# Kernel tuning notes

Measured on AMD Instinct MI355X. Metric: run time of the kernel, lower is better.

## Reference

```python
import jax, jax.numpy as jnp
import numpy as np

HEADS = 16

def setup_inputs() -> dict:
    key = jax.random.key(0)
    ks = jax.random.split(key, 5)
    dim = 1024
    x = jax.random.normal(ks[0], (2, 2048, dim), dtype=jnp.float32)
    scale = 1.0 / np.sqrt(dim)
    Wq = jax.random.normal(ks[1], (dim, dim), dtype=jnp.float32) * scale
    Wk = jax.random.normal(ks[2], (dim, dim), dtype=jnp.float32) * scale
    Wv = jax.random.normal(ks[3], (dim, dim), dtype=jnp.float32) * scale
    Wo = jax.random.normal(ks[4], (dim, dim), dtype=jnp.float32) * scale
    return {"x": x, "Wq": Wq, "Wk": Wk, "Wv": Wv, "Wo": Wo}

def reference(x, Wq, Wk, Wv, Wo):
    b, n, dim = x.shape
    h = HEADS
    d = dim // h
    # projections: torch Linear y = x @ W.T (W is [out,in])
    def split_heads(t):
        return t.reshape(b, n, h, d).transpose(0, 2, 1, 3)  # b h n d
    q = split_heads(x @ Wq.T)
    k = split_heads(x @ Wk.T)
    v = split_heads(x @ Wv.T)
    scale = jnp.asarray(d, x.dtype) ** -0.5
    dots = jnp.einsum('bhid,bhjd->bhij', q, k) * scale
    # causal mask: positions j > i masked (triu with diagonal 1 since i == j)
    i_idx = jnp.arange(n)[:, None]
    j_idx = jnp.arange(n)[None, :]
    mask_value = -jnp.finfo(dots.dtype).max
    dots = jnp.where(j_idx > i_idx, mask_value, dots)
    attn = jax.nn.softmax(dots, axis=-1)  # dropout p=0 (eval) is identity
    out = jnp.einsum('bhij,bhjd->bhid', attn, v)
    out = out.transpose(0, 2, 1, 3).reshape(b, n, dim)
    return out @ Wo.T
```

## Files before the change

kernel.cpp:

```cpp
#include <hip/hip_runtime.h>
#include <hip/hip_bf16.h>

#define BATCH 2
#define SEQ   2048
#define DIM   1024
#define HEADS 16
#define DIMH  64
#define BK    32
#define LOG2E 1.44269504088896340736f
#define SM_SHIFT 16.0f

typedef __attribute__((ext_vector_type(8))) short short8;
typedef __attribute__((ext_vector_type(4))) short short4v;
typedef __attribute__((ext_vector_type(4))) float floatx4;

static __device__ __forceinline__ void gload_lds16(const void* g, void* l) {
    __builtin_amdgcn_global_load_lds(
        (const __attribute__((address_space(1))) void*)g,
        (__attribute__((address_space(3))) void*)l, 16, 0, 0);
}

static __device__ __forceinline__ unsigned pk_trunc(float a, float b) {
    return (__float_as_uint(b) & 0xffff0000u) | (__float_as_uint(a) >> 16);
}

__global__ __launch_bounds__(256) void conv_all(
    const float* __restrict__ x,  const float* __restrict__ Wq,
    const float* __restrict__ Wk, const float* __restrict__ Wv,
    const float* __restrict__ Wo,
    __hip_bfloat16* __restrict__ dst, __hip_bfloat16* __restrict__ dwo)
{
    const size_t NX = (size_t)BATCH * SEQ * DIM;
    const size_t NW = (size_t)DIM * DIM;
    size_t i = ((size_t)blockIdx.x * 256 + threadIdx.x) * 4;
    if (i >= NX + 4 * NW) return;
    const float* src; __hip_bfloat16* d;
    if (i < NX) { src = x + i; d = dst + i; }
    else if (i < NX + 3 * NW) {
        size_t j = i - NX;
        int w = (int)(j >> 20);
        src = ((w == 0) ? Wq : (w == 1) ? Wk : Wv) + (j & (NW - 1));
        d = dst + i;
    } else {
        size_t off = i - (NX + 3 * NW);
        src = Wo + off; d = dwo + off;
    }
    floatx4 f = *reinterpret_cast<const floatx4*>(src);
    short4v o;
    #pragma unroll
    for (int e = 0; e < 4; ++e) {
        __hip_bfloat16 t = __float2bfloat16(f[e]);
        o[e] = *reinterpret_cast<short*>(&t);
    }
    *reinterpret_cast<short4v*>(d) = o;
}

__global__ __launch_bounds__(256) void gemm_qkv(
    const __hip_bfloat16* __restrict__ xbf,
    const __hip_bfloat16* __restrict__ wbf,
    __hip_bfloat16* __restrict__ qkv)
{
    __shared__ __align__(16) short As[2][128 * BK];
    __shared__ __align__(16) short Bs[2][128 * BK];

    const int tid  = threadIdx.x;
    const int wv   = tid >> 6;
    const int lane = tid & 63;
    const int quad = lane >> 4;
    const int l16  = lane & 15;
    const int wm   = wv >> 1, wn = wv & 1;
    const int m0   = blockIdx.x * 128;
    const int n0   = blockIdx.y * 128;
    const int z    = n0 >> 10;
    __hip_bfloat16* out = qkv + (size_t)z * (BATCH * SEQ * DIM);

    const int srow = tid >> 2;
    const int scol = (tid & 3) * 8;

    floatx4 acc[4][4] = {};

#define QSTAGE(buf, k0v) do {                                                       \
    _Pragma("unroll")                                                               \
    for (int i_ = 0; i_ < 2; ++i_) {                                                \
        gload_lds16(xbf + (size_t)(m0 + srow + i_ * 64) * DIM + (k0v) + scol,       \
                    (char*)As[buf] + i_ * 4096 + wv * 1024);                        \
        gload_lds16(wbf + (size_t)(n0 + srow + i_ * 64) * DIM + (k0v) + scol,       \
                    (char*)Bs[buf] + i_ * 4096 + wv * 1024);                        \
    } } while (0)

    QSTAGE(0, 0);
    __syncthreads();

    int cur = 0;
    for (int t = 0; t < DIM / BK; ++t) {
        if (t + 1 < DIM / BK)
            QSTAGE(cur ^ 1, (t + 1) * BK);

        short8 af[4], bf[4];
        #pragma unroll
        for (int mt = 0; mt < 4; ++mt)
            af[mt] = *reinterpret_cast<const short8*>(
                &As[cur][(wm * 64 + mt * 16 + l16) * 32 + quad * 8]);
        #pragma unroll
        for (int nt = 0; nt < 4; ++nt)
            bf[nt] = *reinterpret_cast<const short8*>(
                &Bs[cur][(wn * 64 + nt * 16 + l16) * 32 + quad * 8]);
        #pragma unroll
        for (int mt = 0; mt < 4; ++mt)
            #pragma unroll
            for (int nt = 0; nt < 4; ++nt)
                acc[mt][nt] = __builtin_amdgcn_mfma_f32_16x16x32_bf16(
                    af[mt], bf[nt], acc[mt][nt], 0, 0, 0);

        __syncthreads();
        cur ^= 1;
    }
#undef QSTAGE

    const float esc = (z == 0) ? (0.125f * LOG2E) : 1.0f;
    #pragma unroll
    for (int mt = 0; mt < 4; ++mt) {
        #pragma unroll
        for (int nt = 0; nt < 4; ++nt) {
            const int n  = n0 + wn * 64 + nt * 16 + l16;
            const int hh = (n >> 6) & 15, dv = n & 63;
            #pragma unroll
            for (int r = 0; r < 4; ++r) {
                const int m  = m0 + wm * 64 + mt * 16 + quad * 4 + r;
                const int bb = m >> 11, nn = m & (SEQ - 1);
                const float v = acc[mt][nt][r] * esc;
                if (z < 2)
                    out[((size_t)(bb * HEADS + hh) * SEQ + nn) * DIMH + dv] = __float2bfloat16(v);
                else
                    out[((size_t)(bb * HEADS + hh) * DIMH + dv) * SEQ + nn] = __float2bfloat16(v);
            }
        }
    }
}

__global__ __launch_bounds__(256) void gemm_out(
    const __hip_bfloat16* __restrict__ qhs,
    const __hip_bfloat16* __restrict__ W,
    float* __restrict__ C)
{
    __shared__ __align__(16) short As[2][64 * BK];
    __shared__ __align__(16) short Bs[2][128 * BK];

    const int tid  = threadIdx.x;
    const int wv   = tid >> 6;
    const int lane = tid & 63;
    const int quad = lane >> 4;
    const int l16  = lane & 15;
    const int wn   = wv;
    const int m0   = blockIdx.x * 64;
    const int n0   = blockIdx.y * 128;

    const int srow = tid >> 2;
    const int scol = (tid & 3) * 8;

    floatx4 acc[4][2] = {};

#define OSTAGE(buf, k0v) do {                                                       \
    const int h_    = (k0v) >> 6;                                                   \
    const int koff_ = (k0v) & 63;                                                   \
    const int mA_   = m0 + srow;                                                    \
    const int bbA_  = mA_ >> 11, nnA_ = mA_ & (SEQ - 1);                            \
    gload_lds16(qhs + ((size_t)(bbA_ * HEADS + h_) * SEQ + nnA_) * DIMH + koff_ + scol, \
                (char*)As[buf] + wv * 1024);                                        \
    _Pragma("unroll")                                                               \
    for (int i_ = 0; i_ < 2; ++i_)                                                  \
        gload_lds16(W + (size_t)(n0 + srow + i_ * 64) * DIM + (k0v) + scol,         \
                    (char*)Bs[buf] + i_ * 4096 + wv * 1024);                        \
    } while (0)

    OSTAGE(0, 0);
    __syncthreads();

    int cur = 0;
    for (int t = 0; t < DIM / BK; ++t) {
        if (t + 1 < DIM / BK)
            OSTAGE(cur ^ 1, (t + 1) * BK);

        short8 af[4], bf[2];
        #pragma unroll
        for (int mt = 0; mt < 4; ++mt)
            af[mt] = *reinterpret_cast<const short8*>(
                &As[cur][(mt * 16 + l16) * 32 + quad * 8]);
        #pragma unroll
        for (int nt = 0; nt < 2; ++nt)
            bf[nt] = *reinterpret_cast<const short8*>(
                &Bs[cur][(wn * 32 + nt * 16 + l16) * 32 + quad * 8]);
        #pragma unroll
        for (int mt = 0; mt < 4; ++mt)
            #pragma unroll
            for (int nt = 0; nt < 2; ++nt)
                acc[mt][nt] = __builtin_amdgcn_mfma_f32_16x16x32_bf16(
                    af[mt], bf[nt], acc[mt][nt], 0, 0, 0);

        __syncthreads();
        cur ^= 1;
    }
#undef OSTAGE

    #pragma unroll
    for (int mt = 0; mt < 4; ++mt)
        #pragma unroll
        for (int nt = 0; nt < 2; ++nt) {
            const int n = n0 + wn * 32 + nt * 16 + l16;
            #pragma unroll
            for (int r = 0; r < 4; ++r) {
                const int m = m0 + mt * 16 + quad * 4 + r;
                C[(size_t)m * DIM + n] = acc[mt][nt][r];
            }
        }
}

__global__ __launch_bounds__(256) void attn_causal(
    __hip_bfloat16* __restrict__ qkv)
{
    __shared__ __align__(16) short kt[2][64 * 64];
    __shared__ __align__(16) short vt[2][64 * 64];
    __shared__ __align__(16) short pt[2][2][16 * 72];

    const int id    = blockIdx.x;
    const int combo = id & 31;
    const int p     = id >> 5;
    const int b     = combo >> 4;
    const int h     = combo & 15;
    const int tA = p, tB = 31 - p;
    const int nA = tA + 1;
    const int nB = tB + 1;
    const int total = nA + nB;

    const size_t hoff = (size_t)(b * HEADS + h) * SEQ * DIMH;
    const size_t one  = (size_t)BATCH * SEQ * DIM;
    __hip_bfloat16* qb        = qkv + hoff;
    const __hip_bfloat16* kb  = qkv + one + hoff;
    const __hip_bfloat16* vtg = qkv + 2 * one + hoff;

    const int tid  = threadIdx.x;
    const int wv   = tid >> 6;
    const int g    = wv >> 1;
    const int jh   = wv & 1;
    const int lane = tid & 63;
    const int quad = lane >> 4;
    const int l16  = lane & 15;
    const int xr   = l16 & 7;

    const int crow = tid >> 3;
    const int cjc  = tid & 7;
    const int coff = ((cjc ^ (crow & 7)) * 8);

    const short8 kone8 = {0x3F80, 0x3F80, 0x3F80, 0x3F80,
                          0x3F80, 0x3F80, 0x3F80, 0x3F80};

    int qbase = tA * 64 + g * 16;
    short8 aq[2][2];
    #pragma unroll
    for (int sb = 0; sb < 2; ++sb) {
        aq[sb][0] = *reinterpret_cast<const short8*>(
            qb + (size_t)(qbase + sb * 32 + l16) * DIMH + quad * 8);
        aq[sb][1] = *reinterpret_cast<const short8*>(
            qb + (size_t)(qbase + sb * 32 + l16) * DIMH + 32 + quad * 8);
    }
    floatx4 oacc[2][4] = {};
    floatx4 lsum[2] = {};

    short8 kreg[2], vreg[2];
    #pragma unroll
    for (int i = 0; i < 2; ++i) {
        const int row = crow + 32 * i;
        kreg[i] = *reinterpret_cast<const short8*>(kb + (size_t)row * DIMH + cjc * 8);
        vreg[i] = *reinterpret_cast<const short8*>(vtg + (size_t)row * SEQ + cjc * 8);
    }
    #pragma unroll
    for (int i = 0; i < 2; ++i) {
        const int row = crow + 32 * i;
        *reinterpret_cast<short8*>(&kt[0][row * 64 + coff]) = kreg[i];
        *reinterpret_cast<short8*>(&vt[0][row * 64 + coff]) = vreg[i];
    }
    __syncthreads();

    int cur = 0;
    for (int s = 0; s < total; ++s) {
        const bool lastA = (s == nA - 1);
        const int j0 = ((s < nA) ? s : s - nA) * 64;
        const bool hasn = (s + 1 < total);

        if (hasn) {
            const int s2 = s + 1;
            const int j1 = ((s2 < nA) ? s2 : s2 - nA) * 64;
            #pragma unroll
            for (int i = 0; i < 2; ++i) {
                const int row = crow + 32 * i;
                kreg[i] = *reinterpret_cast<const short8*>(kb + (size_t)(j1 + row) * DIMH + cjc * 8);
                vreg[i] = *reinterpret_cast<const short8*>(vtg + (size_t)row * SEQ + j1 + cjc * 8);
            }
        }

        floatx4 st[2][2];
        #pragma unroll
        for (int tt = 0; tt < 2; ++tt) {
            const int rw = (jh * 2 + tt) * 16 + l16;
            short8 a0 = *reinterpret_cast<const short8*>(&kt[cur][rw * 64 + (quad ^ xr) * 8]);
            short8 a1 = *reinterpret_cast<const short8*>(&kt[cur][rw * 64 + ((quad + 4) ^ xr) * 8]);
            #pragma unroll
            for (int sb = 0; sb < 2; ++sb) {
                floatx4 zz = {};
                zz         = __builtin_amdgcn_mfma_f32_16x16x32_bf16(a0, aq[sb][0], zz, 0, 0, 0);
                st[sb][tt] = __builtin_amdgcn_mfma_f32_16x16x32_bf16(a1, aq[sb][1], zz, 0, 0, 0);
            }
        }

        #pragma unroll
        for (int sb = 0; sb < 2; ++sb) {
            const int qs = qbase + sb * 32;
            if (j0 + 63 > qs) {
                const int qg = qs + l16;
                #pragma unroll
                for (int tt = 0; tt < 2; ++tt)
                    #pragma unroll
                    for (int r = 0; r < 4; ++r) {
                        const int jg = j0 + (jh * 2 + tt) * 16 + quad * 4 + r;
                        if (jg > qg) st[sb][tt][r] = -3.0e38f;
                    }
            }
        }

        #pragma unroll
        for (int sb = 0; sb < 2; ++sb)
            #pragma unroll
            for (int tt = 0; tt < 2; ++tt)
                #pragma unroll
                for (int r = 0; r < 4; ++r)
                    st[sb][tt][r] = __builtin_amdgcn_exp2f(st[sb][tt][r] - SM_SHIFT);

        short8 ph[2];
        #pragma unroll
        for (int sb = 0; sb < 2; ++sb) {
            #pragma unroll
            for (int tt = 0; tt < 2; ++tt) {
                const int t = jh * 2 + tt;
                *reinterpret_cast<unsigned*>(&pt[g][sb][l16 * 72 + t * 16 + quad * 4]) =
                    pk_trunc(st[sb][tt][0], st[sb][tt][1]);
                *reinterpret_cast<unsigned*>(&pt[g][sb][l16 * 72 + t * 16 + quad * 4 + 2]) =
                    pk_trunc(st[sb][tt][2], st[sb][tt][3]);
            }
            ph[sb] = *reinterpret_cast<const short8*>(&pt[g][sb][l16 * 72 + jh * 32 + quad * 8]);
            lsum[sb] = __builtin_amdgcn_mfma_f32_16x16x32_bf16(kone8, ph[sb], lsum[sb], 0, 0, 0);
        }

        #pragma unroll
        for (int dt = 0; dt < 4; ++dt) {
            const int rw = dt * 16 + l16;
            short8 vh = *reinterpret_cast<const short8*>(
                &vt[cur][rw * 64 + ((quad + 4 * jh) ^ xr) * 8]);
            #pragma unroll
            for (int sb = 0; sb < 2; ++sb)
                oacc[sb][dt] = __builtin_amdgcn_mfma_f32_16x16x32_bf16(
                    vh, ph[sb], oacc[sb][dt], 0, 0, 0);
        }

        if (hasn) {
            #pragma unroll
            for (int i = 0; i < 2; ++i) {
                const int row = crow + 32 * i;
                *reinterpret_cast<short8*>(&kt[cur ^ 1][row * 64 + coff]) = kreg[i];
                *reinterpret_cast<short8*>(&vt[cur ^ 1][row * 64 + coff]) = vreg[i];
            }
        }

        if (lastA || s == total - 1) {
            __syncthreads();
            float* xo = reinterpret_cast<float*>(g == 0 ? kt[cur] : vt[cur]);
            float* xl = reinterpret_cast<float*>(pt);
            if (jh == 1) {
                #pragma unroll
                for (int sb = 0; sb < 2; ++sb) {
                    #pragma unroll
                    for (int dt = 0; dt < 4; ++dt)
                        #pragma unroll
                        for (int r = 0; r < 4; ++r)
                            xo[sb * 1024 + (dt * 4 + r) * 64 + lane] = oacc[sb][dt][r];
                    xl[(g * 2 + sb) * 64 + lane] = lsum[sb][0];
                }
            }
            __syncthreads();
            if (jh == 0) {
                #pragma unroll
                for (int sb = 0; sb < 2; ++sb) {
                    const float rl = 1.0f / (lsum[sb][0] + xl[(g * 2 + sb) * 64 + lane]);
                    #pragma unroll
                    for (int dt = 0; dt < 4; ++dt)
                        #pragma unroll
                        for (int r = 0; r < 4; ++r) {
                            const float ov = oacc[sb][dt][r] +
                                             xo[sb * 1024 + (dt * 4 + r) * 64 + lane];
                            qb[(size_t)(qbase + sb * 32 + l16) * DIMH + dt * 16 + quad * 4 + r] =
                                __float2bfloat16(ov * rl);
                        }
                }
            }
            if (lastA) {
                qbase = tB * 64 + g * 16;
                #pragma unroll
                for (int sb = 0; sb < 2; ++sb) {
                    aq[sb][0] = *reinterpret_cast<const short8*>(
                        qb + (size_t)(qbase + sb * 32 + l16) * DIMH + quad * 8);
                    aq[sb][1] = *reinterpret_cast<const short8*>(
                        qb + (size_t)(qbase + sb * 32 + l16) * DIMH + 32 + quad * 8);
                    #pragma unroll
                    for (int dt = 0; dt < 4; ++dt)
                        #pragma unroll
                        for (int r = 0; r < 4; ++r) oacc[sb][dt][r] = 0.f;
                    #pragma unroll
                    for (int r = 0; r < 4; ++r) lsum[sb][r] = 0.f;
                }
            }
        }

        __syncthreads();
        cur ^= 1;
    }
}


extern "C" void kernel_launch(void* const* d_in, const int* in_sizes, int n_in,
                              void* d_out, int out_size, void* d_ws, size_t ws_size,
                              hipStream_t stream) {
    const float* x  = (const float*)d_in[0];
    const float* Wq = (const float*)d_in[1];
    const float* Wk = (const float*)d_in[2];
    const float* Wv = (const float*)d_in[3];
    const float* Wo = (const float*)d_in[4];

    __hip_bfloat16* qkv  = (__hip_bfloat16*)d_ws;
    __hip_bfloat16* wobf = (__hip_bfloat16*)((char*)d_ws + (size_t)24 * 1024 * 1024);

    __hip_bfloat16* xbf = (__hip_bfloat16*)d_out;
    __hip_bfloat16* wbf = xbf + (size_t)BATCH * SEQ * DIM;

    conv_all  <<<8192, 256, 0, stream>>>(x, Wq, Wk, Wv, Wo, xbf, wobf);
    gemm_qkv  <<<dim3((BATCH * SEQ) / 128, (3 * DIM) / 128), 256, 0, stream>>>(xbf, wbf, qkv);
    attn_causal<<<dim3(512), 256, 0, stream>>>(qkv);
    gemm_out  <<<dim3((BATCH * SEQ) / 64, DIM / 128), 256, 0, stream>>>(qkv, wobf, (float*)d_out);
}
```

Before: 187.5 us.

## Split paired causal attention tiles into one block per query tile

The attention kernel previously paired query tiles p and 31-p in one block to balance causal work, processing both sequentially. It now launches one block per query tile (1024 blocks), ordered longest-first, and uses pointer increments for the K/V prefetch addresses. Masking runs only on the diagonal step, and the cross-wave reduction moves out of the loop. This doubles parallelism and removes the mid-loop reset and reload, at the cost of uneven per-block work that relies on the hardware scheduler for balance.

```diff
diff --git a/kernel.cpp b/kernel.cpp
--- a/kernel.cpp
+++ b/kernel.cpp
@@ -224,13 +224,10 @@
 
     const int id    = blockIdx.x;
     const int combo = id & 31;
-    const int p     = id >> 5;
     const int b     = combo >> 4;
     const int h     = combo & 15;
-    const int tA = p, tB = 31 - p;
-    const int nA = tA + 1;
-    const int nB = tB + 1;
-    const int total = nA + nB;
+    const int tile  = 31 - (id >> 5);
+    const int total = tile + 1;
 
     const size_t hoff = (size_t)(b * HEADS + h) * SEQ * DIMH;
     const size_t one  = (size_t)BATCH * SEQ * DIM;
@@ -254,7 +251,7 @@
     const short8 kone8 = {0x3F80, 0x3F80, 0x3F80, 0x3F80,
                           0x3F80, 0x3F80, 0x3F80, 0x3F80};
 
-    int qbase = tA * 64 + g * 16;
+    const int qbase = tile * 64 + g * 16;
     short8 aq[2][2];
     #pragma unroll
     for (int sb = 0; sb < 2; ++sb) {
@@ -266,36 +263,35 @@
     floatx4 oacc[2][4] = {};
     floatx4 lsum[2] = {};
 
+    const __hip_bfloat16* kp0 = kb + (size_t)crow * DIMH + cjc * 8;
+    const __hip_bfloat16* kp1 = kb + (size_t)(crow + 32) * DIMH + cjc * 8;
+    const __hip_bfloat16* vp0 = vtg + (size_t)crow * SEQ + cjc * 8;
+    const __hip_bfloat16* vp1 = vtg + (size_t)(crow + 32) * SEQ + cjc * 8;
+
     short8 kreg[2], vreg[2];
-    #pragma unroll
-    for (int i = 0; i < 2; ++i) {
-        const int row = crow + 32 * i;
-        kreg[i] = *reinterpret_cast<const short8*>(kb + (size_t)row * DIMH + cjc * 8);
-        vreg[i] = *reinterpret_cast<const short8*>(vtg + (size_t)row * SEQ + cjc * 8);
-    }
-    #pragma unroll
-    for (int i = 0; i < 2; ++i) {
-        const int row = crow + 32 * i;
-        *reinterpret_cast<short8*>(&kt[0][row * 64 + coff]) = kreg[i];
-        *reinterpret_cast<short8*>(&vt[0][row * 64 + coff]) = vreg[i];
-    }
+    kreg[0] = *reinterpret_cast<const short8*>(kp0);
+    kreg[1] = *reinterpret_cast<const short8*>(kp1);
+    vreg[0] = *reinterpret_cast<const short8*>(vp0);
+    vreg[1] = *reinterpret_cast<const short8*>(vp1);
+    kp0 += 64 * DIMH; kp1 += 64 * DIMH; vp0 += 64; vp1 += 64;
+
+    *reinterpret_cast<short8*>(&kt[0][crow * 64 + coff])        = kreg[0];
+    *reinterpret_cast<short8*>(&kt[0][(crow + 32) * 64 + coff]) = kreg[1];
+    *reinterpret_cast<short8*>(&vt[0][crow * 64 + coff])        = vreg[0];
+    *reinterpret_cast<short8*>(&vt[0][(crow + 32) * 64 + coff]) = vreg[1];
     __syncthreads();
 
     int cur = 0;
     for (int s = 0; s < total; ++s) {
-        const bool lastA = (s == nA - 1);
-        const int j0 = ((s < nA) ? s : s - nA) * 64;
+        const int j0 = s * 64;
         const bool hasn = (s + 1 < total);
 
         if (hasn) {
-            const int s2 = s + 1;
-            const int j1 = ((s2 < nA) ? s2 : s2 - nA) * 64;
-            #pragma unroll
-            for (int i = 0; i < 2; ++i) {
-                const int row = crow + 32 * i;
-                kreg[i] = *reinterpret_cast<const short8*>(kb + (size_t)(j1 + row) * DIMH + cjc * 8);
-                vreg[i] = *reinterpret_cast<const short8*>(vtg + (size_t)row * SEQ + j1 + cjc * 8);
-            }
+            kreg[0] = *reinterpret_cast<const short8*>(kp0);
+            kreg[1] = *reinterpret_cast<const short8*>(kp1);
+            vreg[0] = *reinterpret_cast<const short8*>(vp0);
+            vreg[1] = *reinterpret_cast<const short8*>(vp1);
+            kp0 += 64 * DIMH; kp1 += 64 * DIMH; vp0 += 64; vp1 += 64;
         }
 
         floatx4 st[2][2];
@@ -312,11 +308,10 @@
             }
         }
 
-        #pragma unroll
-        for (int sb = 0; sb < 2; ++sb) {
-            const int qs = qbase + sb * 32;
-            if (j0 + 63 > qs) {
-                const int qg = qs + l16;
+        if (s == total - 1) {
+            #pragma unroll
+            for (int sb = 0; sb < 2; ++sb) {
+                const int qg = qbase + sb * 32 + l16;
                 #pragma unroll
                 for (int tt = 0; tt < 2; ++tt)
                     #pragma unroll
@@ -362,65 +357,44 @@
         }
 
         if (hasn) {
-            #pragma unroll
-            for (int i = 0; i < 2; ++i) {
-                const int row = crow + 32 * i;
-                *reinterpret_cast<short8*>(&kt[cur ^ 1][row * 64 + coff]) = kreg[i];
-                *reinterpret_cast<short8*>(&vt[cur ^ 1][row * 64 + coff]) = vreg[i];
-            }
-        }
-
-        if (lastA || s == total - 1) {
-            __syncthreads();
-            float* xo = reinterpret_cast<float*>(g == 0 ? kt[cur] : vt[cur]);
-            float* xl = reinterpret_cast<float*>(pt);
-            if (jh == 1) {
-                #pragma unroll
-                for (int sb = 0; sb < 2; ++sb) {
-                    #pragma unroll
-                    for (int dt = 0; dt < 4; ++dt)
-                        #pragma unroll
-                        for (int r = 0; r < 4; ++r)
-                            xo[sb * 1024 + (dt * 4 + r) * 64 + lane] = oacc[sb][dt][r];
-                    xl[(g * 2 + sb) * 64 + lane] = lsum[sb][0];
-                }
-            }
-            __syncthreads();
-            if (jh == 0) {
-                #pragma unroll
-                for (int sb = 0; sb < 2; ++sb) {
-                    const float rl = 1.0f / (lsum[sb][0] + xl[(g * 2 + sb) * 64 + lane]);
-                    #pragma unroll
-                    for (int dt = 0; dt < 4; ++dt)
-                        #pragma unroll
-                        for (int r = 0; r < 4; ++r) {
-                            const float ov = oacc[sb][dt][r] +
-                                             xo[sb * 1024 + (dt * 4 + r) * 64 + lane];
-                            qb[(size_t)(qbase + sb * 32 + l16) * DIMH + dt * 16 + quad * 4 + r] =
-                                __float2bfloat16(ov * rl);
-                        }
-                }
-            }
-            if (lastA) {
-                qbase = tB * 64 + g * 16;
-                #pragma unroll
-                for (int sb = 0; sb < 2; ++sb) {
-                    aq[sb][0] = *reinterpret_cast<const short8*>(
-                        qb + (size_t)(qbase + sb * 32 + l16) * DIMH + quad * 8);
-                    aq[sb][1] = *reinterpret_cast<const short8*>(
-                        qb + (size_t)(qbase + sb * 32 + l16) * DIMH + 32 + quad * 8);
-                    #pragma unroll
-                    for (int dt = 0; dt < 4; ++dt)
-                        #pragma unroll
-                        for (int r = 0; r < 4; ++r) oacc[sb][dt][r] = 0.f;
-                    #pragma unroll
-                    for (int r = 0; r < 4; ++r) lsum[sb][r] = 0.f;
-                }
-            }
+            *reinterpret_cast<short8*>(&kt[cur ^ 1][crow * 64 + coff])        = kreg[0];
+            *reinterpret_cast<short8*>(&kt[cur ^ 1][(crow + 32) * 64 + coff]) = kreg[1];
+            *reinterpret_cast<short8*>(&vt[cur ^ 1][crow * 64 + coff])        = vreg[0];
+            *reinterpret_cast<short8*>(&vt[cur ^ 1][(crow + 32) * 64 + coff]) = vreg[1];
         }
 
         __syncthreads();
         cur ^= 1;
+    }
+
+    float* xo = reinterpret_cast<float*>(g == 0 ? kt[0] : vt[0]);
+    float* xl = reinterpret_cast<float*>(pt);
+    if (jh == 1) {
+        #pragma unroll
+        for (int sb = 0; sb < 2; ++sb) {
+            #pragma unroll
+            for (int dt = 0; dt < 4; ++dt)
+                #pragma unroll
+                for (int r = 0; r < 4; ++r)
+                    xo[sb * 1024 + (dt * 4 + r) * 64 + lane] = oacc[sb][dt][r];
+            xl[(g * 2 + sb) * 64 + lane] = lsum[sb][0];
+        }
+    }
+    __syncthreads();
+    if (jh == 0) {
+        #pragma unroll
+        for (int sb = 0; sb < 2; ++sb) {
+            const float rl = 1.0f / (lsum[sb][0] + xl[(g * 2 + sb) * 64 + lane]);
+            #pragma unroll
+            for (int dt = 0; dt < 4; ++dt)
+                #pragma unroll
+                for (int r = 0; r < 4; ++r) {
+                    const float ov = oacc[sb][dt][r] +
+                                     xo[sb * 1024 + (dt * 4 + r) * 64 + lane];
+                    qb[(size_t)(qbase + sb * 32 + l16) * DIMH + dt * 16 + quad * 4 + r] =
+                        __float2bfloat16(ov * rl);
+                }
+        }
     }
 }
 
@@ -442,6 +416,6 @@
 
     conv_all  <<<8192, 256, 0, stream>>>(x, Wq, Wk, Wv, Wo, xbf, wobf);
     gemm_qkv  <<<dim3((BATCH * SEQ) / 128, (3 * DIM) / 128), 256, 0, stream>>>(xbf, wbf, qkv);
-    attn_causal<<<dim3(512), 256, 0, stream>>>(qkv);
+    attn_causal<<<dim3(1024), 256, 0, stream>>>(qkv);
     gemm_out  <<<dim3((BATCH * SEQ) / 64, DIM / 128), 256, 0, stream>>>(qkv, wobf, (float*)d_out);
 }
```

Result: faster. 182.5 us, median of 2 (-2.7%).
